# Performance work log

Measured on AMD Instinct MI355X. Metric: run time of the kernel, lower is better.

Reference implementation:

```python
import jax, jax.numpy as jnp
import numpy as np

B, K, D = 2, 2048, 1024
H, DQ, DV = 16, 64, 64
DFF = 4096
ATT_SIZE = 256
LN_EPS = 1e-5


def _layernorm(x, g, b):
    mu = jnp.mean(x, axis=-1, keepdims=True)
    var = jnp.mean(jnp.square(x - mu), axis=-1, keepdims=True)
    return (x - mu) * jax.lax.rsqrt(var + LN_EPS) * g + b


def setup_inputs() -> dict:
    key = jax.random.key(0)
    ks = jax.random.split(key, 16)
    s = lambda d: 1.0 / np.sqrt(d)
    return {
        "x": jax.random.normal(ks[0], (B, K, D), dtype=jnp.float32),
        "Wq": jax.random.normal(ks[1], (D, H * DQ), dtype=jnp.float32) * s(D),
        "bq": jnp.zeros((H * DQ,), dtype=jnp.float32),
        "Wk": jax.random.normal(ks[2], (D, H * DQ), dtype=jnp.float32) * s(D),
        "bk": jnp.zeros((H * DQ,), dtype=jnp.float32),
        "Wv": jax.random.normal(ks[3], (D, H * DV), dtype=jnp.float32) * s(D),
        "bv": jnp.zeros((H * DV,), dtype=jnp.float32),
        "Wo": jax.random.normal(ks[4], (H * DV, D), dtype=jnp.float32) * s(H * DV),
        "bo": jnp.zeros((D,), dtype=jnp.float32),
        "W1": jax.random.normal(ks[5], (D, DFF), dtype=jnp.float32) * s(D),
        "b1": jnp.zeros((DFF,), dtype=jnp.float32),
        "W2": jax.random.normal(ks[6], (DFF, D), dtype=jnp.float32) * s(DFF),
        "b2": jnp.zeros((D,), dtype=jnp.float32),
        "ln1_g": jnp.ones((D,), dtype=jnp.float32),
        "ln1_b": jnp.zeros((D,), dtype=jnp.float32),
        "ln2_g": jnp.ones((D,), dtype=jnp.float32),
        "ln2_b": jnp.zeros((D,), dtype=jnp.float32),
    }


def reference(x, Wq, bq, Wk, bk, Wv, bv, Wo, bo, W1, b1, W2, b2,
              ln1_g, ln1_b, ln2_g, ln2_b):
    b, k, d = x.shape
    # --- multi-head attention (heads formed by chunking last dim) ---
    q = (x @ Wq + bq).reshape(b, k, H, DQ)  # [b,k,h,dq]
    kk = (x @ Wk + bk).reshape(b, k, H, DQ)
    v = (x @ Wv + bv).reshape(b, k, H, DV)
    # NOTE: original scales by sqrt(K) (sequence length), not sqrt(d_q)
    scores = jnp.einsum('bshd,bthd->bhst', q, kk) / jnp.sqrt(jnp.float32(k))
    idx = jnp.arange(k)
    band_mask = jnp.abs(idx[:, None] - idx[None, :]) > ATT_SIZE  # [k,k] bool
    scores = jnp.where(band_mask[None, None], -jnp.inf, scores)
    attn = jax.nn.softmax(scores, axis=-1)
    ctx = jnp.einsum('bhst,bthd->bshd', attn, v).reshape(b, k, H * DV)
    sa = ctx @ Wo + bo
    x1 = _layernorm(sa + x, ln1_g, ln1_b)
    # --- position-wise FFN (exact GELU as torch F.gelu default) ---
    ff = (jax.nn.gelu(x1 @ W1 + b1, approximate=False)) @ W2 + b2
    return _layernorm(ff + x1, ln2_g, ln2_b)
```

## Files before the change

kernel.cpp:

```cpp
#include <hip/hip_runtime.h>
#include <cstdint>
#include <math.h>

typedef unsigned short u16;
typedef __attribute__((ext_vector_type(8))) short bf16x8;
typedef __attribute__((ext_vector_type(4))) float f32x4;

#define DEVI __device__ __forceinline__

DEVI u16 f2bf(float f) {
  union { float f; uint32_t u; } v; v.f = f;
  return (u16)((v.u + 0x7FFFu + ((v.u >> 16) & 1u)) >> 16);
}
DEVI float bf2f(u16 h) {
  union { uint32_t u; float f; } v; v.u = ((uint32_t)h) << 16;
  return v.f;
}

DEVI void gload16(const void* g, void* l) {
  __builtin_amdgcn_global_load_lds(
      (const __attribute__((address_space(1))) void*)g,
      (__attribute__((address_space(3))) void*)l, 16, 0, 0);
}

DEVI float gelu_fast(float u) {
  float u2 = u * u;
  float t = __builtin_fmaf(0.044715f * u2, u, u);
  float e = __expf(1.5957691216057308f * t);
  float r = __builtin_amdgcn_rcpf(1.0f + e);
  return u - u * r;
}

DEVI void tcvt_body(const float* __restrict__ W, u16* __restrict__ Wt,
                    int Kd, int N, int n0, int k0, float* t) {
  const int r = threadIdx.x >> 4, c4 = (threadIdx.x & 15) * 4;
#pragma unroll
  for (int p = 0; p < 4; ++p) {
    int row = p * 16 + r;
    float4 f = *(const float4*)(W + (size_t)(k0 + row) * N + n0 + c4);
    *(float4*)&t[row * 68 + c4] = f;
  }
  __syncthreads();
#pragma unroll
  for (int p = 0; p < 4; ++p) {
    int n = p * 16 + r;
    float v0 = t[(c4 + 0) * 68 + n];
    float v1 = t[(c4 + 1) * 68 + n];
    float v2 = t[(c4 + 2) * 68 + n];
    float v3 = t[(c4 + 3) * 68 + n];
    uint32_t lo = (uint32_t)f2bf(v0) | ((uint32_t)f2bf(v1) << 16);
    uint32_t hi = (uint32_t)f2bf(v2) | ((uint32_t)f2bf(v3) << 16);
    *(uint2*)(Wt + (size_t)(n0 + n) * Kd + k0 + c4) = make_uint2(lo, hi);
  }
}

__global__ __launch_bounds__(256)
void prep_kernel(const float* __restrict__ Wq, const float* __restrict__ Wk,
                 const float* __restrict__ Wv, const float* __restrict__ Wo,
                 const float* __restrict__ W1, const float* __restrict__ W2,
                 const float* __restrict__ x, const float* __restrict__ bq,
                 const float* __restrict__ bk, const float* __restrict__ bv,
                 u16* __restrict__ WqkvT, u16* __restrict__ WoT,
                 u16* __restrict__ W1T, u16* __restrict__ W2T,
                 u16* __restrict__ xb, float* __restrict__ bqkv)
{
  __shared__ float t[64 * 68];
  const int b = blockIdx.x;
  if (b < 1024) {
    int wsel = b >> 8, tt = b & 255;
    const float* W = (wsel == 0) ? Wq : (wsel == 1) ? Wk : (wsel == 2) ? Wv : Wo;
    u16* dst = (wsel == 3) ? WoT : WqkvT + (size_t)wsel * 1024 * 1024;
    tcvt_body(W, dst, 1024, 1024, (tt & 15) * 64, (tt >> 4) * 64, t);
  } else if (b < 2048) {
    int tt = b - 1024;
    tcvt_body(W1, W1T, 1024, 4096, (tt & 63) * 64, (tt >> 6) * 64, t);
  } else if (b < 3072) {
    int tt = b - 2048;
    tcvt_body(W2, W2T, 4096, 1024, (tt & 15) * 64, (tt >> 4) * 64, t);
  } else if (b < 7168) {
    int i = ((b - 3072) * 256 + threadIdx.x) * 4;
    float4 f = *(const float4*)(x + i);
    uint32_t lo = (uint32_t)f2bf(f.x) | ((uint32_t)f2bf(f.y) << 16);
    uint32_t hi = (uint32_t)f2bf(f.z) | ((uint32_t)f2bf(f.w) << 16);
    *(uint2*)(xb + i) = make_uint2(lo, hi);
  } else {
    int i = (b - 7168) * 256 + threadIdx.x;
    const float* s = (i < 1024) ? bq : ((i < 2048) ? bk : bv);
    bqkv[i] = s[i & 1023];
  }
}

template<int MODE>
__global__ __launch_bounds__(256, 4)
void gemm_kernel(const u16* __restrict__ A, const u16* __restrict__ Bt,
                 const float* __restrict__ bias, void* __restrict__ C0,
                 void* __restrict__ C1, int N, int Kfull, int Kpart)
{
  __shared__ u16 As0[128 * 32], As1[128 * 32];
  __shared__ u16 Bs0[128 * 32], Bs1[128 * 32];
  const int tid = threadIdx.x;
  const int nbx = gridDim.x, nby = gridDim.y;
  int lin = blockIdx.y * nbx + blockIdx.x;
  int band = lin / (8 * nbx);
  int rem = lin - band * (8 * nbx);
  int gsz = min(nby - band * 8, 8);
  const int m0 = (band * 8 + rem % gsz) * 128;
  const int n0 = (rem / gsz) * 128;
  const int kbase = (MODE == 2) ? (int)blockIdx.z * Kpart : 0;
  const int w = tid >> 6, lane = tid & 63;
  const int wm = (w >> 1) * 64, wn = (w & 1) * 64;
  const int mr = lane & 15, ko = (lane >> 4) * 8;
  const int rq = (lane >> 4) * 4;
  const int w32 = w * 32;

  f32x4 acc[4][4];
#pragma unroll
  for (int i = 0; i < 4; ++i)
#pragma unroll
    for (int j = 0; j < 4; ++j) {
      f32x4 z = {0.f, 0.f, 0.f, 0.f};
      acc[i][j] = z;
    }

  const int lr = lane >> 2, lk = (lane & 3) * 8;
  const u16* aG = A  + (size_t)(m0 + w32 + lr) * Kfull + kbase + lk;
  const u16* bG = Bt + (size_t)(n0 + w32 + lr) * Kfull + kbase + lk;
  u16* aD00 = &As0[(w32 +  0) * 32];
  u16* aD01 = &As0[(w32 + 16) * 32];
  u16* aD10 = &As1[(w32 +  0) * 32];
  u16* aD11 = &As1[(w32 + 16) * 32];
  u16* bD00 = &Bs0[(w32 +  0) * 32];
  u16* bD01 = &Bs0[(w32 + 16) * 32];
  u16* bD10 = &Bs1[(w32 +  0) * 32];
  u16* bD11 = &Bs1[(w32 + 16) * 32];
  const size_t row16 = (size_t)16 * Kfull;

  for (int k0 = 0; k0 < Kpart; k0 += 64) {
    gload16(aG + k0,              aD00);
    gload16(aG + row16 + k0,      aD01);
    gload16(aG + k0 + 32,         aD10);
    gload16(aG + row16 + k0 + 32, aD11);
    gload16(bG + k0,              bD00);
    gload16(bG + row16 + k0,      bD01);
    gload16(bG + k0 + 32,         bD10);
    gload16(bG + row16 + k0 + 32, bD11);
    __syncthreads();
#pragma unroll
    for (int s = 0; s < 2; ++s) {
      const u16* Ap = s ? As1 : As0;
      const u16* Bp = s ? Bs1 : Bs0;
      bf16x8 af[4], bf[4];
#pragma unroll
      for (int i = 0; i < 4; ++i)
        af[i] = *(const bf16x8*)&Ap[(wm + i * 16 + mr) * 32 + ko];
#pragma unroll
      for (int j = 0; j < 4; ++j)
        bf[j] = *(const bf16x8*)&Bp[(wn + j * 16 + mr) * 32 + ko];
#pragma unroll
      for (int i = 0; i < 4; ++i)
#pragma unroll
        for (int j = 0; j < 4; ++j)
          acc[i][j] = __builtin_amdgcn_mfma_f32_16x16x32_bf16(bf[j], af[i], acc[i][j], 0, 0, 0);
    }
    __syncthreads();
  }

  {
    const bool part1 = (MODE == 2) && (blockIdx.z == 1);
#pragma unroll
    for (int i = 0; i < 4; ++i) {
      size_t mrow = (size_t)(m0 + wm + i * 16 + mr) * N;
#pragma unroll
      for (int j = 0; j < 4; ++j) {
        int nb = n0 + wn + j * 16 + rq;
        float v0 = acc[i][j][0], v1 = acc[i][j][1];
        float v2 = acc[i][j][2], v3 = acc[i][j][3];
        if (!part1) {
          float4 b4 = *(const float4*)&bias[nb];
          v0 += b4.x; v1 += b4.y; v2 += b4.z; v3 += b4.w;
        }
        if (MODE == 1) {
          v0 = gelu_fast(v0); v1 = gelu_fast(v1);
          v2 = gelu_fast(v2); v3 = gelu_fast(v3);
        }
        uint32_t lo = (uint32_t)f2bf(v0) | ((uint32_t)f2bf(v1) << 16);
        uint32_t hi = (uint32_t)f2bf(v2) | ((uint32_t)f2bf(v3) << 16);
        u16* dst = part1 ? (u16*)C1 : (u16*)C0;
        *(uint2*)(dst + mrow + nb) = make_uint2(lo, hi);
      }
    }
  }
}

#define VMW4 asm volatile("s_waitcnt vmcnt(4)" ::: "memory")
#define VMW2 asm volatile("s_waitcnt vmcnt(2)" ::: "memory")
#define VMW0 asm volatile("s_waitcnt vmcnt(0)" ::: "memory")
#define VMWN

DEVI void stage_half(const u16* __restrict__ G, int row0, int Kfull, int tk,
                     u16* lds_half, int w, int srow, int scol) {
  const u16* s = G + (size_t)(row0 + w * 8 + srow) * Kfull + tk + scol;
  u16* d = lds_half + w * 512;
  gload16(s, d);
  gload16(s + ((size_t)Kfull << 6), d + 4096);
}

#define PH(MH, NH, WAIT) do {                                                 \
    const u16* Ab_ = &As[(cur * 2 + (MH)) * 8192];                            \
    const u16* Bb_ = &Bs[(cur * 2 + (NH)) * 8192];                            \
    bf16x8 a0_[4], a1_[4], b0_[2], b1_[2];                                    \
    _Pragma("unroll")                                                         \
    for (int i_ = 0; i_ < 4; ++i_) {                                          \
      const u16* p_ = Ab_ + (wm * 64 + i_ * 16 + mr) * 64;                    \
      a0_[i_] = *(const bf16x8*)(p_ + c0);                                    \
      a1_[i_] = *(const bf16x8*)(p_ + c1);                                    \
    }                                                                         \
    _Pragma("unroll")                                                         \
    for (int j_ = 0; j_ < 2; ++j_) {                                          \
      const u16* p_ = Bb_ + (wn * 32 + j_ * 16 + mr) * 64;                    \
      b0_[j_] = *(const bf16x8*)(p_ + c0);                                    \
      b1_[j_] = *(const bf16x8*)(p_ + c1);                                    \
    }                                                                         \
    __builtin_amdgcn_s_barrier();                                             \
    __builtin_amdgcn_s_setprio(1);                                            \
    _Pragma("unroll")                                                         \
    for (int i_ = 0; i_ < 4; ++i_)                                            \
      _Pragma("unroll")                                                       \
      for (int j_ = 0; j_ < 2; ++j_) {                                        \
        acc[(MH)*4+i_][(NH)*2+j_] = __builtin_amdgcn_mfma_f32_16x16x32_bf16(  \
            b0_[j_], a0_[i_], acc[(MH)*4+i_][(NH)*2+j_], 0, 0, 0);            \
        acc[(MH)*4+i_][(NH)*2+j_] = __builtin_amdgcn_mfma_f32_16x16x32_bf16(  \
            b1_[j_], a1_[i_], acc[(MH)*4+i_][(NH)*2+j_], 0, 0, 0);            \
      }                                                                       \
    __builtin_amdgcn_s_setprio(0);                                            \
    WAIT;                                                                     \
    __builtin_amdgcn_s_barrier();                                             \
  } while (0)

template<int MODE>
__global__ __launch_bounds__(512, 2)
void gemm256_kernel(const u16* __restrict__ A, const u16* __restrict__ Bt,
                    const float* __restrict__ bias, void* __restrict__ C0,
                    void* __restrict__ C1, int N, int Kfull, int NBN)
{
  __shared__ u16 As[32768];
  __shared__ u16 Bs[32768];
  const int tid = threadIdx.x;
  const int w = tid >> 6, lane = tid & 63;
  const int wm = w >> 2, wn = w & 3;
  const int mr = lane & 15;
  const int rq = (lane >> 4) * 4;

  const int lin = blockIdx.x;
  const int q = gridDim.x >> 3;
  const int wg = (lin & 7) * q + (lin >> 3);
  const int mt = wg / NBN, nt = wg - mt * NBN;
  const int m0 = mt * 256, n0 = nt * 256;

  const int srow = lane >> 3;
  const int scol = ((lane & 7) ^ srow) << 3;
  const int bl = (lane >> 4) << 4;
  const int sw = (mr & 7) << 4;
  const int c0 = (bl ^ sw) >> 1;
  const int c1 = ((64 + bl) ^ sw) >> 1;

  f32x4 acc[8][4];
#pragma unroll
  for (int i = 0; i < 8; ++i)
#pragma unroll
    for (int j = 0; j < 4; ++j) {
      f32x4 z = {0.f, 0.f, 0.f, 0.f};
      acc[i][j] = z;
    }

  const int NT = Kfull >> 6;

  stage_half(A,  m0 + 0,   Kfull, 0, &As[0],    w, srow, scol);
  stage_half(Bt, n0 + 0,   Kfull, 0, &Bs[0],    w, srow, scol);
  stage_half(Bt, n0 + 128, Kfull, 0, &Bs[8192], w, srow, scol);
  stage_half(A,  m0 + 128, Kfull, 0, &As[8192], w, srow, scol);
  VMW4;
  __builtin_amdgcn_s_barrier();

  int t = 0;
  for (; t < NT - 1; ++t) {
    const int cur = t & 1, nxt = cur ^ 1, k1 = (t + 1) * 64;
    stage_half(A,  m0 + 0,   Kfull, k1, &As[(nxt*2+0)*8192], w, srow, scol);
    PH(0, 0, VMW4);
    stage_half(Bt, n0 + 0,   Kfull, k1, &Bs[(nxt*2+0)*8192], w, srow, scol);
    PH(0, 1, VMW4);
    stage_half(Bt, n0 + 128, Kfull, k1, &Bs[(nxt*2+1)*8192], w, srow, scol);
    PH(1, 1, VMW4);
    stage_half(A,  m0 + 128, Kfull, k1, &As[(nxt*2+1)*8192], w, srow, scol);
    PH(1, 0, VMW4);
  }
  {
    const int cur = t & 1;
    PH(0, 0, VMW2);
    PH(0, 1, VMW0);
    PH(1, 1, VMWN);
    PH(1, 0, VMWN);
  }

  if (MODE == 0) {
    if (n0 < 2048) {
#pragma unroll
      for (int mi = 0; mi < 8; ++mi) {
        int mg = m0 + (mi >> 2) * 128 + wm * 64 + (mi & 3) * 16 + mr;
        size_t mrow = (size_t)mg * 2048;
#pragma unroll
        for (int ni = 0; ni < 4; ++ni) {
          int ng = n0 + (ni >> 1) * 128 + wn * 32 + (ni & 1) * 16 + rq;
          float4 b4 = *(const float4*)&bias[ng];
          f32x4 a = acc[mi][ni];
          uint32_t lo = (uint32_t)f2bf(a[0] + b4.x) | ((uint32_t)f2bf(a[1] + b4.y) << 16);
          uint32_t hi = (uint32_t)f2bf(a[2] + b4.z) | ((uint32_t)f2bf(a[3] + b4.w) << 16);
          *(uint2*)((u16*)C0 + mrow + ng) = make_uint2(lo, hi);
        }
      }
    } else {
#pragma unroll
      for (int mi = 0; mi < 8; ++mi) {
        int mg = m0 + (mi >> 2) * 128 + wm * 64 + (mi & 3) * 16 + mr;
#pragma unroll
        for (int ni = 0; ni < 4; ++ni) {
          int ng = n0 + (ni >> 1) * 128 + wn * 32 + (ni & 1) * 16 + rq;
          float4 b4 = *(const float4*)&bias[ng];
          f32x4 a = acc[mi][ni];
          int d = ng - 2048;
          ((u16*)C1)[(size_t)(d + 0) * 4096 + mg] = f2bf(a[0] + b4.x);
          ((u16*)C1)[(size_t)(d + 1) * 4096 + mg] = f2bf(a[1] + b4.y);
          ((u16*)C1)[(size_t)(d + 2) * 4096 + mg] = f2bf(a[2] + b4.z);
          ((u16*)C1)[(size_t)(d + 3) * 4096 + mg] = f2bf(a[3] + b4.w);
        }
      }
    }
  } else {
#pragma unroll
    for (int mi = 0; mi < 8; ++mi) {
      int mg = m0 + (mi >> 2) * 128 + wm * 64 + (mi & 3) * 16 + mr;
      size_t mrow = (size_t)mg * N;
#pragma unroll
      for (int ni = 0; ni < 4; ++ni) {
        int ng = n0 + (ni >> 1) * 128 + wn * 32 + (ni & 1) * 16 + rq;
        float4 b4 = *(const float4*)&bias[ng];
        f32x4 a = acc[mi][ni];
        float v0 = gelu_fast(a[0] + b4.x), v1 = gelu_fast(a[1] + b4.y);
        float v2 = gelu_fast(a[2] + b4.z), v3 = gelu_fast(a[3] + b4.w);
        uint32_t lo = (uint32_t)f2bf(v0) | ((uint32_t)f2bf(v1) << 16);
        uint32_t hi = (uint32_t)f2bf(v2) | ((uint32_t)f2bf(v3) << 16);
        *(uint2*)((u16*)C0 + mrow + ng) = make_uint2(lo, hi);
      }
    }
  }
}

__global__ __launch_bounds__(256)
void attn_kernel(const u16* __restrict__ QKb, const u16* __restrict__ Vt,
                 u16* __restrict__ ctx)
{
  const int KS = 2048, HD = 1024;
  __shared__ u16 Qs[64 * 80];
  __shared__ u16 Ks[64 * 80];
  __shared__ u16 Vts[64 * 72];
  __shared__ u16 Ps[64 * 72];

  const int qt = blockIdx.x, hh = blockIdx.y, bb = blockIdx.z;
  const int s0 = qt * 64;
  const int tid = threadIdx.x, w = tid >> 6, lane = tid & 63;
  const int mr = lane & 15, ko = (lane >> 4) * 8, rq = (lane >> 4) * 4;
  const int sr = tid >> 3, sc = (tid & 7) * 8;
  const int vrow = tid >> 2, vtc = (tid & 3) * 16;
  const float qsc = 0.022097086912079608f;
  const int qg = s0 + w * 16 + mr;

#pragma unroll
  for (int p = 0; p < 2; ++p) {
    int row = p * 32 + sr;
    uint4 u = *(const uint4*)(QKb + (size_t)(bb * KS + s0 + row) * 2048 + hh * 64 + sc);
    *(uint4*)&Qs[row * 80 + sc] = u;
  }

  f32x4 accO[4];
#pragma unroll
  for (int j = 0; j < 4; ++j) { f32x4 z = {0.f,0.f,0.f,0.f}; accO[j] = z; }
  float lsum = 0.f;

  for (int c = 0; c < 9; ++c) {
    int tb = s0 - 256 + c * 64;
    if (tb < 0 || tb >= KS) continue;
    __syncthreads();
#pragma unroll
    for (int p = 0; p < 2; ++p) {
      int row = p * 32 + sr;
      uint4 uk = *(const uint4*)(QKb + (size_t)(bb * KS + tb + row) * 2048 + 1024 + hh * 64 + sc);
      *(uint4*)&Ks[row * 80 + sc] = uk;
    }
    {
      const u16* vsrc = Vt + (size_t)(hh * 64 + vrow) * 4096 + bb * KS + tb + vtc;
      *(uint4*)&Vts[vrow * 72 + vtc]     = *(const uint4*)vsrc;
      *(uint4*)&Vts[vrow * 72 + vtc + 8] = *(const uint4*)(vsrc + 8);
    }
    __syncthreads();

    f32x4 sacc[4];
#pragma unroll
    for (int j = 0; j < 4; ++j) { f32x4 z = {0.f,0.f,0.f,0.f}; sacc[j] = z; }
#pragma unroll
    for (int s = 0; s < 2; ++s) {
      bf16x8 aq = *(const bf16x8*)&Qs[(w * 16 + mr) * 80 + s * 32 + ko];
#pragma unroll
      for (int j = 0; j < 4; ++j) {
        bf16x8 bk = *(const bf16x8*)&Ks[(j * 16 + mr) * 80 + s * 32 + ko];
        sacc[j] = __builtin_amdgcn_mfma_f32_16x16x32_bf16(bk, aq, sacc[j], 0, 0, 0);
      }
    }

#pragma unroll
    for (int j = 0; j < 4; ++j) {
      int tgb = tb + j * 16 + rq;
      float p0, p1, p2, p3;
      {
        int d0 = qg - tgb;
        float s_ = sacc[j][0] * qsc;
        p0 = (d0 > 256 || d0 < -256) ? 0.f : __expf(s_);
        int d1 = d0 - 1; s_ = sacc[j][1] * qsc;
        p1 = (d1 > 256 || d1 < -256) ? 0.f : __expf(s_);
        int d2 = d0 - 2; s_ = sacc[j][2] * qsc;
        p2 = (d2 > 256 || d2 < -256) ? 0.f : __expf(s_);
        int d3 = d0 - 3; s_ = sacc[j][3] * qsc;
        p3 = (d3 > 256 || d3 < -256) ? 0.f : __expf(s_);
      }
      lsum += p0 + p1 + p2 + p3;
      uint32_t lo = (uint32_t)f2bf(p0) | ((uint32_t)f2bf(p1) << 16);
      uint32_t hi = (uint32_t)f2bf(p2) | ((uint32_t)f2bf(p3) << 16);
      *(uint2*)&Ps[(w * 16 + mr) * 72 + j * 16 + rq] = make_uint2(lo, hi);
    }
#pragma unroll
    for (int s = 0; s < 2; ++s) {
      bf16x8 ap = *(const bf16x8*)&Ps[(w * 16 + mr) * 72 + s * 32 + ko];
#pragma unroll
      for (int j = 0; j < 4; ++j) {
        bf16x8 bv = *(const bf16x8*)&Vts[(j * 16 + mr) * 72 + s * 32 + ko];
        accO[j] = __builtin_amdgcn_mfma_f32_16x16x32_bf16(bv, ap, accO[j], 0, 0, 0);
      }
    }
  }

  float l = lsum;
  l += __shfl_xor(l, 16, 64);
  l += __shfl_xor(l, 32, 64);
  float inv = 1.f / l;
  size_t base = (size_t)(bb * KS + qg) * HD + hh * 64;
#pragma unroll
  for (int j = 0; j < 4; ++j) {
    uint32_t lo = (uint32_t)f2bf(accO[j][0] * inv) | ((uint32_t)f2bf(accO[j][1] * inv) << 16);
    uint32_t hi = (uint32_t)f2bf(accO[j][2] * inv) | ((uint32_t)f2bf(accO[j][3] * inv) << 16);
    *(uint2*)(ctx + base + j * 16 + rq) = make_uint2(lo, hi);
  }
}

DEVI void bfadd4(const u16* p, size_t base, float& v0, float& v1, float& v2, float& v3) {
  uint2 u = *(const uint2*)(p + base);
  v0 += bf2f((u16)(u.x & 0xFFFFu));
  v1 += bf2f((u16)(u.x >> 16));
  v2 += bf2f((u16)(u.y & 0xFFFFu));
  v3 += bf2f((u16)(u.y >> 16));
}

template<int OUT32>
__global__ __launch_bounds__(256)
void ln_kernel(const u16* __restrict__ p0, const u16* __restrict__ p1,
               const u16* __restrict__ res, const float* __restrict__ g,
               const float* __restrict__ be, void* __restrict__ out)
{
  __shared__ float red[8];
  const int row = blockIdx.x, tid = threadIdx.x;
  const int w = tid >> 6, lane = tid & 63;
  size_t base = (size_t)row * 1024 + tid * 4;
  float v0 = 0.f, v1 = 0.f, v2 = 0.f, v3 = 0.f;
  bfadd4(p0, base, v0, v1, v2, v3);
  bfadd4(p1, base, v0, v1, v2, v3);
  bfadd4(res, base, v0, v1, v2, v3);
  float s1 = v0 + v1 + v2 + v3;
  float s2 = v0 * v0 + v1 * v1 + v2 * v2 + v3 * v3;
#pragma unroll
  for (int o = 32; o > 0; o >>= 1) {
    s1 += __shfl_xor(s1, o, 64);
    s2 += __shfl_xor(s2, o, 64);
  }
  if (lane == 0) { red[w] = s1; red[4 + w] = s2; }
  __syncthreads();
  s1 = red[0] + red[1] + red[2] + red[3];
  s2 = red[4] + red[5] + red[6] + red[7];
  float mu = s1 * (1.f / 1024.f);
  float var = s2 * (1.f / 1024.f) - mu * mu;
  float rs = rsqrtf(var + 1e-5f);
  float4 gv = *(const float4*)(g + tid * 4);
  float4 bv = *(const float4*)(be + tid * 4);
  float o0 = (v0 - mu) * rs * gv.x + bv.x;
  float o1 = (v1 - mu) * rs * gv.y + bv.y;
  float o2 = (v2 - mu) * rs * gv.z + bv.z;
  float o3 = (v3 - mu) * rs * gv.w + bv.w;
  if (OUT32) {
    float4 ov; ov.x = o0; ov.y = o1; ov.z = o2; ov.w = o3;
    *(float4*)((float*)out + base) = ov;
  } else {
    uint32_t lo = (uint32_t)f2bf(o0) | ((uint32_t)f2bf(o1) << 16);
    uint32_t hi = (uint32_t)f2bf(o2) | ((uint32_t)f2bf(o3) << 16);
    *(uint2*)((u16*)out + base) = make_uint2(lo, hi);
  }
}

extern "C" void kernel_launch(void* const* d_in, const int* in_sizes, int n_in,
                              void* d_out, int out_size, void* d_ws, size_t ws_size,
                              hipStream_t stream)
{
  (void)in_sizes; (void)n_in; (void)out_size; (void)ws_size;
  const float* x   = (const float*)d_in[0];
  const float* Wq  = (const float*)d_in[1];
  const float* bq  = (const float*)d_in[2];
  const float* Wk  = (const float*)d_in[3];
  const float* bk  = (const float*)d_in[4];
  const float* Wv  = (const float*)d_in[5];
  const float* bv  = (const float*)d_in[6];
  const float* Wo  = (const float*)d_in[7];
  const float* bo  = (const float*)d_in[8];
  const float* W1  = (const float*)d_in[9];
  const float* b1  = (const float*)d_in[10];
  const float* W2  = (const float*)d_in[11];
  const float* b2  = (const float*)d_in[12];
  const float* g1  = (const float*)d_in[13];
  const float* be1 = (const float*)d_in[14];
  const float* g2  = (const float*)d_in[15];
  const float* be2 = (const float*)d_in[16];

  char* ws = (char*)d_ws;
  const size_t MB = 1048576;
  u16*   W1T   = (u16*)(ws + 0 * MB);
  u16*   Y0b   = (u16*)(ws + 0 * MB);
  u16*   xb    = (u16*)(ws + 8 * MB);
  u16*   Y1b   = (u16*)(ws + 8 * MB);
  u16*   WqkvT = (u16*)(ws + 16 * MB);
  u16*   X1b   = (u16*)(ws + 16 * MB);
  u16*   WoT   = (u16*)(ws + 22 * MB);
  u16*   QKb   = (u16*)(ws + 24 * MB);
  u16*   SA0b  = (u16*)(ws + 24 * MB);
  u16*   SA1b  = (u16*)(ws + 32 * MB);
  u16*   Hb    = (u16*)(ws + 24 * MB);
  u16*   Vt    = (u16*)(ws + 40 * MB);
  float* bqkv  = (float*)(ws + 48 * MB);
  u16*   Cb    = (u16*)(ws + 48 * MB);
  u16*   W2T   = (u16*)(ws + 56 * MB);
  float* yout  = (float*)d_out;

  dim3 blk(256);
  dim3 blk512(512);
  prep_kernel<<<7180, blk, 0, stream>>>(Wq, Wk, Wv, Wo, W1, W2, x, bq, bk, bv,
                                        WqkvT, WoT, W1T, W2T, xb, bqkv);
  gemm256_kernel<0><<<dim3(192), blk512, 0, stream>>>(xb, WqkvT, bqkv, QKb, Vt, 3072, 1024, 12);
  attn_kernel<<<dim3(32, 16, 2), blk, 0, stream>>>(QKb, Vt, Cb);
  gemm_kernel<2><<<dim3(8, 32, 2), blk, 0, stream>>>(Cb, WoT, bo, SA0b, SA1b, 1024, 1024, 512);
  ln_kernel<0><<<4096, blk, 0, stream>>>(SA0b, SA1b, xb, g1, be1, X1b);
  gemm256_kernel<1><<<dim3(256), blk512, 0, stream>>>(X1b, W1T, b1, Hb, nullptr, 4096, 1024, 16);
  gemm_kernel<2><<<dim3(8, 32, 2), blk, 0, stream>>>(Hb, W2T, b2, Y0b, Y1b, 1024, 4096, 2048);
  ln_kernel<1><<<4096, blk, 0, stream>>>(Y0b, Y1b, X1b, g2, be2, yout);
}
```

Measured before the change: 339.5 us.

## Reuse A/B register fragments across GEMM sub-phases and regroup global staging

Restructures the 256x256 GEMM main loop so LDS fragments for A and B halves are loaded once into registers and reused across the four MFMA quadrants, instead of reloading both A and B for every quadrant. The four global-to-LDS stage_half calls are regrouped into two pairs per tile, and the wait/barrier points are reorganized. This reduces LDS read traffic by about a third but raises register pressure (holds aF plus two B fragment sets), which could hurt occupancy at 512 threads x2 blocks. The changed vmcnt waits may alter how well memory loads overlap with compute.

```diff
diff --git a/kernel.cpp b/kernel.cpp
--- a/kernel.cpp
+++ b/kernel.cpp
@@ -193,9 +193,10 @@
 }
 
 #define VMW4 asm volatile("s_waitcnt vmcnt(4)" ::: "memory")
-#define VMW2 asm volatile("s_waitcnt vmcnt(2)" ::: "memory")
 #define VMW0 asm volatile("s_waitcnt vmcnt(0)" ::: "memory")
-#define VMWN
+#define BAR  __builtin_amdgcn_s_barrier()
+#define PRI1 __builtin_amdgcn_s_setprio(1)
+#define PRI0 __builtin_amdgcn_s_setprio(0)
 
 DEVI void stage_half(const u16* __restrict__ G, int row0, int Kfull, int tk,
                      u16* lds_half, int w, int srow, int scol) {
@@ -205,36 +206,58 @@
   gload16(s + ((size_t)Kfull << 6), d + 4096);
 }
 
-#define PH(MH, NH, WAIT) do {                                                 \
-    const u16* Ab_ = &As[(cur * 2 + (MH)) * 8192];                            \
-    const u16* Bb_ = &Bs[(cur * 2 + (NH)) * 8192];                            \
-    bf16x8 a0_[4], a1_[4], b0_[2], b1_[2];                                    \
-    _Pragma("unroll")                                                         \
-    for (int i_ = 0; i_ < 4; ++i_) {                                          \
-      const u16* p_ = Ab_ + (wm * 64 + i_ * 16 + mr) * 64;                    \
-      a0_[i_] = *(const bf16x8*)(p_ + c0);                                    \
-      a1_[i_] = *(const bf16x8*)(p_ + c1);                                    \
-    }                                                                         \
+#define LDA(BASE, HALF)                                                       \
+  _Pragma("unroll")                                                           \
+  for (int i_ = 0; i_ < 4; ++i_) {                                            \
+    const u16* p_ = (BASE) + (HALF) * 8192 + (wm * 64 + i_ * 16 + mr) * 64;   \
+    aF[i_][0] = *(const bf16x8*)(p_ + c0);                                    \
+    aF[i_][1] = *(const bf16x8*)(p_ + c1);                                    \
+  }
+
+#define LDB(BASE, HALF, DST)                                                  \
+  _Pragma("unroll")                                                           \
+  for (int j_ = 0; j_ < 2; ++j_) {                                            \
+    const u16* p_ = (BASE) + (HALF) * 8192 + (wn * 32 + j_ * 16 + mr) * 64;   \
+    DST[j_][0] = *(const bf16x8*)(p_ + c0);                                   \
+    DST[j_][1] = *(const bf16x8*)(p_ + c1);                                   \
+  }
+
+#define MM(MH, NH, BF)                                                        \
+  _Pragma("unroll")                                                           \
+  for (int i_ = 0; i_ < 4; ++i_)                                              \
     _Pragma("unroll")                                                         \
     for (int j_ = 0; j_ < 2; ++j_) {                                          \
-      const u16* p_ = Bb_ + (wn * 32 + j_ * 16 + mr) * 64;                    \
-      b0_[j_] = *(const bf16x8*)(p_ + c0);                                    \
-      b1_[j_] = *(const bf16x8*)(p_ + c1);                                    \
+      acc[(MH)*4+i_][(NH)*2+j_] = __builtin_amdgcn_mfma_f32_16x16x32_bf16(    \
+          BF[j_][0], aF[i_][0], acc[(MH)*4+i_][(NH)*2+j_], 0, 0, 0);          \
+      acc[(MH)*4+i_][(NH)*2+j_] = __builtin_amdgcn_mfma_f32_16x16x32_bf16(    \
+          BF[j_][1], aF[i_][1], acc[(MH)*4+i_][(NH)*2+j_], 0, 0, 0);          \
+    }
+
+#define TILE(DO_STAGE, W1END, W4END) do {                                     \
+    const int cur_ = t & 1, nxt_ = cur_ ^ 1;                                  \
+    const int k1_ = (t + 1) << 6;                                             \
+    const u16* Ac_ = &As[cur_ * 16384];                                       \
+    const u16* Bc_ = &Bs[cur_ * 16384];                                       \
+                                       \
+    if (DO_STAGE) {                                                           \
+      stage_half(A,  m0,       Kfull, k1_, &As[nxt_ * 16384], w, srow, scol); \
+      stage_half(Bt, n0,       Kfull, k1_, &Bs[nxt_ * 16384], w, srow, scol); \
     }                                                                         \
-    __builtin_amdgcn_s_barrier();                                             \
-    __builtin_amdgcn_s_setprio(1);                                            \
-    _Pragma("unroll")                                                         \
-    for (int i_ = 0; i_ < 4; ++i_)                                            \
-      _Pragma("unroll")                                                       \
-      for (int j_ = 0; j_ < 2; ++j_) {                                        \
-        acc[(MH)*4+i_][(NH)*2+j_] = __builtin_amdgcn_mfma_f32_16x16x32_bf16(  \
-            b0_[j_], a0_[i_], acc[(MH)*4+i_][(NH)*2+j_], 0, 0, 0);            \
-        acc[(MH)*4+i_][(NH)*2+j_] = __builtin_amdgcn_mfma_f32_16x16x32_bf16(  \
-            b1_[j_], a1_[i_], acc[(MH)*4+i_][(NH)*2+j_], 0, 0, 0);            \
-      }                                                                       \
-    __builtin_amdgcn_s_setprio(0);                                            \
-    WAIT;                                                                     \
-    __builtin_amdgcn_s_barrier();                                             \
+    LDA(Ac_, 0);                                                              \
+    LDB(Bc_, 0, bF0);                                                         \
+    BAR; PRI1; MM(0, 0, bF0); PRI0; W1END; BAR;                               \
+                                       \
+    if (DO_STAGE) {                                                           \
+      stage_half(Bt, n0 + 128, Kfull, k1_, &Bs[nxt_ * 16384 + 8192], w, srow, scol); \
+      stage_half(A,  m0 + 128, Kfull, k1_, &As[nxt_ * 16384 + 8192], w, srow, scol); \
+    }                                                                         \
+    LDB(Bc_, 1, bF1);                                                         \
+    BAR; PRI1; MM(0, 1, bF1); PRI0; BAR;                                      \
+                                       \
+    LDA(Ac_, 1);                                                              \
+    BAR; PRI1; MM(1, 1, bF1); PRI0; BAR;                                      \
+                        \
+    BAR; PRI1; MM(1, 0, bF0); PRI0; W4END; BAR;                               \
   } while (0)
 
 template<int MODE>
@@ -273,34 +296,22 @@
       acc[i][j] = z;
     }
 
+  bf16x8 aF[4][2], bF0[2][2], bF1[2][2];
+
   const int NT = Kfull >> 6;
 
-  stage_half(A,  m0 + 0,   Kfull, 0, &As[0],    w, srow, scol);
-  stage_half(Bt, n0 + 0,   Kfull, 0, &Bs[0],    w, srow, scol);
+  stage_half(A,  m0,       Kfull, 0, &As[0],    w, srow, scol);
+  stage_half(Bt, n0,       Kfull, 0, &Bs[0],    w, srow, scol);
   stage_half(Bt, n0 + 128, Kfull, 0, &Bs[8192], w, srow, scol);
   stage_half(A,  m0 + 128, Kfull, 0, &As[8192], w, srow, scol);
   VMW4;
-  __builtin_amdgcn_s_barrier();
+  BAR;
 
   int t = 0;
   for (; t < NT - 1; ++t) {
-    const int cur = t & 1, nxt = cur ^ 1, k1 = (t + 1) * 64;
-    stage_half(A,  m0 + 0,   Kfull, k1, &As[(nxt*2+0)*8192], w, srow, scol);
-    PH(0, 0, VMW4);
-    stage_half(Bt, n0 + 0,   Kfull, k1, &Bs[(nxt*2+0)*8192], w, srow, scol);
-    PH(0, 1, VMW4);
-    stage_half(Bt, n0 + 128, Kfull, k1, &Bs[(nxt*2+1)*8192], w, srow, scol);
-    PH(1, 1, VMW4);
-    stage_half(A,  m0 + 128, Kfull, k1, &As[(nxt*2+1)*8192], w, srow, scol);
-    PH(1, 0, VMW4);
-  }
-  {
-    const int cur = t & 1;
-    PH(0, 0, VMW2);
-    PH(0, 1, VMW0);
-    PH(1, 1, VMWN);
-    PH(1, 0, VMWN);
-  }
+    TILE(1, VMW4, VMW4);
+  }
+  TILE(0, VMW0, (void)0);
 
   if (MODE == 0) {
     if (n0 < 2048) {
```

After: 325.9 us. 4.0% less time.

## Restructure 256x256 GEMM mainloop into 4-slot K=32 pipeline with 3-deep prefetch

Applied to the files above, without the earlier changes.

Replaces the double-buffered K=64 mainloop, which had four quarter-phases each with two barriers, with a 4-slot ring of K=32 tiles prefetched three stages ahead and one barrier per step. Each wave now owns a contiguous 128x64 sub-tile and issues 32 MFMAs per step from one batch of LDS fragment loads, with a new XOR swizzle suited to the 32-wide rows. The aim is deeper overlap of global loads with compute and fewer barriers per K element. In exchange each step carries less compute to hide latency behind, and the new swizzle may cause more LDS bank conflicts.

```diff
diff --git a/kernel.cpp b/kernel.cpp
--- a/kernel.cpp
+++ b/kernel.cpp
@@ -192,50 +192,21 @@
   }
 }
 
+#define VMW8 asm volatile("s_waitcnt vmcnt(8)" ::: "memory")
 #define VMW4 asm volatile("s_waitcnt vmcnt(4)" ::: "memory")
-#define VMW2 asm volatile("s_waitcnt vmcnt(2)" ::: "memory")
 #define VMW0 asm volatile("s_waitcnt vmcnt(0)" ::: "memory")
-#define VMWN
-
-DEVI void stage_half(const u16* __restrict__ G, int row0, int Kfull, int tk,
-                     u16* lds_half, int w, int srow, int scol) {
-  const u16* s = G + (size_t)(row0 + w * 8 + srow) * Kfull + tk + scol;
-  u16* d = lds_half + w * 512;
-  gload16(s, d);
-  gload16(s + ((size_t)Kfull << 6), d + 4096);
-}
-
-#define PH(MH, NH, WAIT) do {                                                 \
-    const u16* Ab_ = &As[(cur * 2 + (MH)) * 8192];                            \
-    const u16* Bb_ = &Bs[(cur * 2 + (NH)) * 8192];                            \
-    bf16x8 a0_[4], a1_[4], b0_[2], b1_[2];                                    \
-    _Pragma("unroll")                                                         \
-    for (int i_ = 0; i_ < 4; ++i_) {                                          \
-      const u16* p_ = Ab_ + (wm * 64 + i_ * 16 + mr) * 64;                    \
-      a0_[i_] = *(const bf16x8*)(p_ + c0);                                    \
-      a1_[i_] = *(const bf16x8*)(p_ + c1);                                    \
-    }                                                                         \
-    _Pragma("unroll")                                                         \
-    for (int j_ = 0; j_ < 2; ++j_) {                                          \
-      const u16* p_ = Bb_ + (wn * 32 + j_ * 16 + mr) * 64;                    \
-      b0_[j_] = *(const bf16x8*)(p_ + c0);                                    \
-      b1_[j_] = *(const bf16x8*)(p_ + c1);                                    \
-    }                                                                         \
-    __builtin_amdgcn_s_barrier();                                             \
-    __builtin_amdgcn_s_setprio(1);                                            \
-    _Pragma("unroll")                                                         \
-    for (int i_ = 0; i_ < 4; ++i_)                                            \
-      _Pragma("unroll")                                                       \
-      for (int j_ = 0; j_ < 2; ++j_) {                                        \
-        acc[(MH)*4+i_][(NH)*2+j_] = __builtin_amdgcn_mfma_f32_16x16x32_bf16(  \
-            b0_[j_], a0_[i_], acc[(MH)*4+i_][(NH)*2+j_], 0, 0, 0);            \
-        acc[(MH)*4+i_][(NH)*2+j_] = __builtin_amdgcn_mfma_f32_16x16x32_bf16(  \
-            b1_[j_], a1_[i_], acc[(MH)*4+i_][(NH)*2+j_], 0, 0, 0);            \
-      }                                                                       \
-    __builtin_amdgcn_s_setprio(0);                                            \
-    WAIT;                                                                     \
-    __builtin_amdgcn_s_barrier();                                             \
-  } while (0)
+#define BAR  __builtin_amdgcn_s_barrier()
+#define PRI1 __builtin_amdgcn_s_setprio(1)
+#define PRI0 __builtin_amdgcn_s_setprio(0)
+
+DEVI void stage32(const u16* __restrict__ G, int row0, int Kfull, int kk,
+                  u16* slotbase, int w, int lane) {
+  const int r = w * 16 + (lane >> 2);
+  const int c = (((lane & 3) ^ ((lane >> 3) & 3)) << 3);
+  const u16* s = G + (size_t)(row0 + r) * Kfull + kk + c;
+  gload16(s, slotbase + w * 512);
+  gload16(s + ((size_t)Kfull << 7), slotbase + 4096 + w * 512);
+}
 
 template<int MODE>
 __global__ __launch_bounds__(512, 2)
@@ -243,8 +214,8 @@
                     const float* __restrict__ bias, void* __restrict__ C0,
                     void* __restrict__ C1, int N, int Kfull, int NBN)
 {
-  __shared__ u16 As[32768];
-  __shared__ u16 Bs[32768];
+  __shared__ u16 As[4 * 8192];
+  __shared__ u16 Bs[4 * 8192];
   const int tid = threadIdx.x;
   const int w = tid >> 6, lane = tid & 63;
   const int wm = w >> 2, wn = w & 3;
@@ -257,12 +228,7 @@
   const int mt = wg / NBN, nt = wg - mt * NBN;
   const int m0 = mt * 256, n0 = nt * 256;
 
-  const int srow = lane >> 3;
-  const int scol = ((lane & 7) ^ srow) << 3;
-  const int bl = (lane >> 4) << 4;
-  const int sw = (mr & 7) << 4;
-  const int c0 = (bl ^ sw) >> 1;
-  const int c1 = ((64 + bl) ^ sw) >> 1;
+  const int sc2 = (((lane >> 4) ^ ((mr >> 1) & 3)) << 3);
 
   f32x4 acc[8][4];
 #pragma unroll
@@ -273,44 +239,64 @@
       acc[i][j] = z;
     }
 
-  const int NT = Kfull >> 6;
-
-  stage_half(A,  m0 + 0,   Kfull, 0, &As[0],    w, srow, scol);
-  stage_half(Bt, n0 + 0,   Kfull, 0, &Bs[0],    w, srow, scol);
-  stage_half(Bt, n0 + 128, Kfull, 0, &Bs[8192], w, srow, scol);
-  stage_half(A,  m0 + 128, Kfull, 0, &As[8192], w, srow, scol);
-  VMW4;
-  __builtin_amdgcn_s_barrier();
-
-  int t = 0;
-  for (; t < NT - 1; ++t) {
-    const int cur = t & 1, nxt = cur ^ 1, k1 = (t + 1) * 64;
-    stage_half(A,  m0 + 0,   Kfull, k1, &As[(nxt*2+0)*8192], w, srow, scol);
-    PH(0, 0, VMW4);
-    stage_half(Bt, n0 + 0,   Kfull, k1, &Bs[(nxt*2+0)*8192], w, srow, scol);
-    PH(0, 1, VMW4);
-    stage_half(Bt, n0 + 128, Kfull, k1, &Bs[(nxt*2+1)*8192], w, srow, scol);
-    PH(1, 1, VMW4);
-    stage_half(A,  m0 + 128, Kfull, k1, &As[(nxt*2+1)*8192], w, srow, scol);
-    PH(1, 0, VMW4);
-  }
-  {
-    const int cur = t & 1;
-    PH(0, 0, VMW2);
-    PH(0, 1, VMW0);
-    PH(1, 1, VMWN);
-    PH(1, 0, VMWN);
-  }
+  const int NT = Kfull >> 5;
+
+  stage32(A,  m0, Kfull,  0, &As[0],        w, lane);
+  stage32(Bt, n0, Kfull,  0, &Bs[0],        w, lane);
+  stage32(A,  m0, Kfull, 32, &As[8192],     w, lane);
+  stage32(Bt, n0, Kfull, 32, &Bs[8192],     w, lane);
+  stage32(A,  m0, Kfull, 64, &As[2 * 8192], w, lane);
+  stage32(Bt, n0, Kfull, 64, &Bs[2 * 8192], w, lane);
+  VMW8;
+  BAR;
+
+#define STEP32(ST, DO_STAGE, WAIT) do {                                       \
+    const int sl_ = (ST) & 3;                                                 \
+    const u16* Ap_ = &As[sl_ * 8192];                                         \
+    const u16* Bp_ = &Bs[sl_ * 8192];                                         \
+    if (DO_STAGE) {                                                           \
+      const int kk_ = ((ST) + 3) << 5;                                        \
+      const int ns_ = ((ST) + 3) & 3;                                         \
+      stage32(A,  m0, Kfull, kk_, &As[ns_ * 8192], w, lane);                  \
+      stage32(Bt, n0, Kfull, kk_, &Bs[ns_ * 8192], w, lane);                  \
+    }                                                                         \
+    bf16x8 aF[8], bF[4];                                                      \
+    _Pragma("unroll")                                                         \
+    for (int i_ = 0; i_ < 8; ++i_)                                            \
+      aF[i_] = *(const bf16x8*)&Ap_[(wm * 128 + i_ * 16 + mr) * 32 + sc2];    \
+    _Pragma("unroll")                                                         \
+    for (int j_ = 0; j_ < 4; ++j_)                                            \
+      bF[j_] = *(const bf16x8*)&Bp_[(wn * 64 + j_ * 16 + mr) * 32 + sc2];     \
+    PRI1;                                                                     \
+    _Pragma("unroll")                                                         \
+    for (int i_ = 0; i_ < 8; ++i_)                                            \
+      _Pragma("unroll")                                                       \
+      for (int j_ = 0; j_ < 4; ++j_)                                          \
+        acc[i_][j_] = __builtin_amdgcn_mfma_f32_16x16x32_bf16(                \
+            bF[j_], aF[i_], acc[i_][j_], 0, 0, 0);                            \
+    PRI0;                                                                     \
+    WAIT;                                                                     \
+  } while (0)
+
+  int st = 0;
+  for (; st < NT - 3; ++st) {
+    STEP32(st, 1, VMW8);
+    BAR;
+  }
+  STEP32(st, 0, VMW4); BAR; ++st;
+  STEP32(st, 0, VMW0); BAR; ++st;
+  STEP32(st, 0, (void)0);
+#undef STEP32
 
   if (MODE == 0) {
     if (n0 < 2048) {
 #pragma unroll
       for (int mi = 0; mi < 8; ++mi) {
-        int mg = m0 + (mi >> 2) * 128 + wm * 64 + (mi & 3) * 16 + mr;
+        int mg = m0 + wm * 128 + mi * 16 + mr;
         size_t mrow = (size_t)mg * 2048;
 #pragma unroll
         for (int ni = 0; ni < 4; ++ni) {
-          int ng = n0 + (ni >> 1) * 128 + wn * 32 + (ni & 1) * 16 + rq;
+          int ng = n0 + wn * 64 + ni * 16 + rq;
           float4 b4 = *(const float4*)&bias[ng];
           f32x4 a = acc[mi][ni];
           uint32_t lo = (uint32_t)f2bf(a[0] + b4.x) | ((uint32_t)f2bf(a[1] + b4.y) << 16);
@@ -321,10 +307,10 @@
     } else {
 #pragma unroll
       for (int mi = 0; mi < 8; ++mi) {
-        int mg = m0 + (mi >> 2) * 128 + wm * 64 + (mi & 3) * 16 + mr;
+        int mg = m0 + wm * 128 + mi * 16 + mr;
 #pragma unroll
         for (int ni = 0; ni < 4; ++ni) {
-          int ng = n0 + (ni >> 1) * 128 + wn * 32 + (ni & 1) * 16 + rq;
+          int ng = n0 + wn * 64 + ni * 16 + rq;
           float4 b4 = *(const float4*)&bias[ng];
           f32x4 a = acc[mi][ni];
           int d = ng - 2048;
@@ -338,11 +324,11 @@
   } else {
 #pragma unroll
     for (int mi = 0; mi < 8; ++mi) {
-      int mg = m0 + (mi >> 2) * 128 + wm * 64 + (mi & 3) * 16 + mr;
+      int mg = m0 + wm * 128 + mi * 16 + mr;
       size_t mrow = (size_t)mg * N;
 #pragma unroll
       for (int ni = 0; ni < 4; ++ni) {
-        int ng = n0 + (ni >> 1) * 128 + wn * 32 + (ni & 1) * 16 + rq;
+        int ng = n0 + wn * 64 + ni * 16 + rq;
         float4 b4 = *(const float4*)&bias[ng];
         f32x4 a = acc[mi][ni];
         float v0 = gelu_fast(a[0] + b4.x), v1 = gelu_fast(a[1] + b4.y);
```

Result: faster. 327.5 us (-3.5%).
